# Optimization experiments

Measured on AMD Instinct MI355X. Metric: run time of the kernel, lower is better.

Reference implementation:

```python
import jax, jax.numpy as jnp
import numpy as np

B, L, D, H = 4, 2048, 512, 8
HD = D // H  # 64
MAX_REL = 4


def setup_inputs() -> dict:
    key = jax.random.key(0)
    ks = jax.random.split(key, 13)
    s = 1.0 / np.sqrt(D)
    return {
        "q": jax.random.normal(ks[0], (B, L, D), jnp.float32),
        "k": jax.random.normal(ks[1], (B, L, D), jnp.float32),
        "v": jax.random.normal(ks[2], (B, L, D), jnp.float32),
        "Wq": jax.random.normal(ks[3], (D, D), jnp.float32) * s,
        "bq": jax.random.normal(ks[4], (D,), jnp.float32) * 0.01,
        "Wk": jax.random.normal(ks[5], (D, D), jnp.float32) * s,
        "bk": jax.random.normal(ks[6], (D,), jnp.float32) * 0.01,
        "Wv": jax.random.normal(ks[7], (D, D), jnp.float32) * s,
        "bv": jax.random.normal(ks[8], (D,), jnp.float32) * 0.01,
        "Wo": jax.random.normal(ks[9], (D, D), jnp.float32) * s,
        "bo": jax.random.normal(ks[10], (D,), jnp.float32) * 0.01,
        "rel_k_table": jax.random.normal(ks[11], (2 * MAX_REL + 1, HD), jnp.float32),
        "rel_v_table": jax.random.normal(ks[12], (2 * MAX_REL + 1, HD), jnp.float32),
    }


def _to_heads(x):
    # [B, L, D] -> [B, H, L, HD]
    b, l, d = x.shape
    return x.reshape(b, l, H, d // H).transpose(0, 2, 1, 3)


def reference(q, k, v, Wq, bq, Wk, bk, Wv, bv, Wo, bo, rel_k_table, rel_v_table):
    # NOTE: in the source, the relative-attention output is overwritten by the
    # plain SDPA call immediately after, so observable math = SDPA only.
    # rel_k_table / rel_v_table are dead parameters (zero gradient).
    relu = jax.nn.relu
    qh = _to_heads(relu(q @ Wq.T + bq))  # [B,H,L,HD]
    kh = _to_heads(relu(k @ Wk.T + bk))
    vh = _to_heads(relu(v @ Wv.T + bv))
    # scale by sqrt(d_key)=sqrt(512), matching the original (not sqrt(head_dim))
    scores = jnp.einsum("bhqd,bhkd->bhqk", qh, kh) / jnp.sqrt(jnp.float32(D))
    attn = jax.nn.softmax(scores, axis=-1)
    out = jnp.einsum("bhqk,bhkd->bhqd", attn, vh)  # [B,H,L,HD]
    out = out.transpose(0, 2, 1, 3).reshape(B, L, D)
    return relu(out @ Wo.T + bo)
```

## Files before the change

kernel.cpp:

```cpp
#include <hip/hip_runtime.h>
#include <hip/hip_bf16.h>

#define B_  4
#define L_  2048
#define D_  512
#define H_  8
#define HD_ 64
#define M_  (B_ * L_)

typedef __bf16 bf16;
typedef __attribute__((ext_vector_type(8)))  __bf16 bf16x8;
typedef __attribute__((ext_vector_type(4)))  __bf16 bf16x4;
typedef __attribute__((ext_vector_type(16))) float  f32x16;

__device__ __forceinline__ f32x16 mfma32(bf16x8 a, bf16x8 b, f32x16 c) {
    return __builtin_amdgcn_mfma_f32_32x32x16_bf16(a, b, c, 0, 0, 0);
}

__device__ __forceinline__ void pack_body(const float* __restrict__ src,
                                          bf16* __restrict__ dst, int R,
                                          int m0, int k0)
{
    __shared__ __align__(16) bf16 tile[64][76];
    const int t = threadIdx.x;
#pragma unroll
    for (int rep = 0; rep < 4; rep++) {
        const int idx = rep * 256 + t;
        const int r = idx >> 4, c4 = idx & 15;
        const float4 f = *(const float4*)(src + (size_t)(m0 + r) * 512 + k0 + c4 * 4);
        bf16x4 v; v[0] = (bf16)f.x; v[1] = (bf16)f.y; v[2] = (bf16)f.z; v[3] = (bf16)f.w;
        *(bf16x4*)(&tile[r][c4 * 4]) = v;
    }
    __syncthreads();
#pragma unroll
    for (int rep = 0; rep < 2; rep++) {
        const int s = rep * 256 + t;
        const int ml = s & 63, kpl = s >> 6;
        const bf16x4 lo = *(const bf16x4*)(&tile[ml][kpl * 8]);
        const bf16x4 hi4 = *(const bf16x4*)(&tile[ml][kpl * 8 + 4]);
        bf16x8 v;
#pragma unroll
        for (int e = 0; e < 4; e++) { v[e] = lo[e]; v[e + 4] = hi4[e]; }
        *(bf16x8*)(dst + ((size_t)(k0 / 8 + kpl) * R + m0 + ml) * 8) = v;
    }
}

__global__ __launch_bounds__(256) void pack_all(
    const float* __restrict__ q, const float* __restrict__ k,
    const float* __restrict__ W0, const float* __restrict__ W1,
    const float* __restrict__ W2, const float* __restrict__ W3,
    bf16* __restrict__ Wp, bf16* __restrict__ P0, bf16* __restrict__ P1)
{
    const int z = blockIdx.z;
    if (z < 4) {
        if (blockIdx.x >= 8) return;
        const float* src = z == 0 ? W0 : z == 1 ? W1 : z == 2 ? W2 : W3;
        pack_body(src, Wp + (size_t)z * 64 * 512 * 8, 512, blockIdx.x * 64, blockIdx.y * 64);
    } else {
        pack_body(z == 4 ? q : k, z == 4 ? P0 : P1, M_, blockIdx.x * 64, blockIdx.y * 64);
    }
}

__global__ __launch_bounds__(256) void pack_x(const float* __restrict__ src,
                                              bf16* __restrict__ dst)
{
    pack_body(src, dst, M_, blockIdx.x * 64, blockIdx.y * 64);
}

struct PJob {
    const bf16* X; const bf16* W; const float* bias; void* out;
    float postmul; int mode;
};

__global__ __launch_bounds__(256) void proj_kernel(PJob j0, PJob j1)
{
    const PJob jb = (blockIdx.z == 0) ? j0 : j1;
    const int w    = threadIdx.x >> 6;
    const int lane = threadIdx.x & 63;
    const int l31  = lane & 31;
    const int hi   = lane >> 5;
    const int m0 = blockIdx.x * 128;
    const int n0 = blockIdx.y * 64;
    const int mh = w & 1;
    const int nh = w >> 1;

    __shared__ __align__(16) bf16 Ab[2][16][64][8];
    __shared__ __align__(16) bf16 Bb[2][8][64][8];

    f32x16 acc[2];
#pragma unroll
    for (int mi = 0; mi < 2; mi++)
#pragma unroll
        for (int r = 0; r < 16; r++) acc[mi][r] = 0.0f;

    auto ldA = [&](int f, int k0) -> bf16x8 {
        return *(const bf16x8*)(jb.X + ((size_t)((k0 >> 3) + (f >> 2) * 2 + hi) * M_
                                        + m0 + (f & 3) * 32 + l31) * 8);
    };
    auto ldB = [&](int f, int k0) -> bf16x8 {
        return *(const bf16x8*)(jb.W + ((size_t)((k0 >> 3) + (f >> 1) * 2 + hi) * 512
                                        + n0 + (f & 1) * 32 + l31) * 8);
    };

    bf16x8 ra[4], rb[2];
#pragma unroll
    for (int i = 0; i < 4; i++) ra[i] = ldA(w * 4 + i, 0);
#pragma unroll
    for (int i = 0; i < 2; i++) rb[i] = ldB(w * 2 + i, 0);
#pragma unroll
    for (int i = 0; i < 4; i++) *(bf16x8*)(&Ab[0][w * 4 + i][lane][0]) = ra[i];
#pragma unroll
    for (int i = 0; i < 2; i++) *(bf16x8*)(&Bb[0][w * 2 + i][lane][0]) = rb[i];
    __syncthreads();

    for (int it = 0; it < 8; it++) {
        const int cur = it & 1;
        if (it < 7) {
            const int kn = (it + 1) * 64;
#pragma unroll
            for (int i = 0; i < 4; i++) ra[i] = ldA(w * 4 + i, kn);
#pragma unroll
            for (int i = 0; i < 2; i++) rb[i] = ldB(w * 2 + i, kn);
        }
#pragma unroll
        for (int ks = 0; ks < 4; ks++) {
            const bf16x8 bfr = *(const bf16x8*)(&Bb[cur][ks * 2 + nh][lane][0]);
#pragma unroll
            for (int mi = 0; mi < 2; mi++) {
                const bf16x8 afr = *(const bf16x8*)(&Ab[cur][ks * 4 + mh * 2 + mi][lane][0]);
                acc[mi] = mfma32(afr, bfr, acc[mi]);
            }
        }
        if (it < 7) {
#pragma unroll
            for (int i = 0; i < 4; i++) *(bf16x8*)(&Ab[1 - cur][w * 4 + i][lane][0]) = ra[i];
#pragma unroll
            for (int i = 0; i < 2; i++) *(bf16x8*)(&Bb[1 - cur][w * 2 + i][lane][0]) = rb[i];
            __syncthreads();
        }
    }

    const int col = n0 + nh * 32 + l31;
    const float bn = jb.bias[col];
    const int mode = jb.mode;
#pragma unroll
    for (int mi = 0; mi < 2; mi++)
#pragma unroll
        for (int r = 0; r < 16; r++) {
            const int row = m0 + (mh * 2 + mi) * 32 + (r & 3) + 8 * (r >> 2) + 4 * hi;
            float v = fmaxf(acc[mi][r] + bn, 0.0f);
            if (mode == 2) {
                ((float*)jb.out)[(size_t)row * D_ + col] = v;
            } else {
                v *= jb.postmul;
                const int b = row >> 11, l = row & (L_ - 1);
                const int h = col >> 6,  hd = col & (HD_ - 1);
                const int bh = b * H_ + h;
                size_t idx;
                if (mode == 0) {
                    idx = ((size_t)bh * L_ + l) * HD_ + hd;
                } else if (mode == 1) {
                    idx = (((size_t)bh * 8 + (hd >> 3)) * L_ + l) * 8 + (hd & 7);
                } else {
                    const int swzl = (l & ~15) | (l & 3) | ((l & 4) << 1) | ((l & 8) >> 1);
                    idx = (((size_t)bh * 256 + (swzl >> 3)) * 64 + hd) * 8 + (swzl & 7);
                }
                ((bf16*)jb.out)[idx] = (bf16)v;
            }
        }
}

__global__ __launch_bounds__(128) void attn_kernel(
    const bf16* __restrict__ qh, const bf16* __restrict__ Kp,
    const bf16* __restrict__ Vp, bf16* __restrict__ Op)
{
    const int w    = threadIdx.x >> 6;
    const int lane = threadIdx.x & 63;
    const int l31  = lane & 31;
    const int hi   = lane >> 5;
    const int bh   = blockIdx.y;
    const int qb   = blockIdx.x * 64 + w * 32;

    const bf16* Q   = qh + (size_t)bh * L_ * HD_;
    const bf16* Kpb = Kp + (size_t)bh * 8 * L_ * 8;
    const bf16* Vpb = Vp + (size_t)bh * 256 * 64 * 8;

    __shared__ __align__(16) bf16 Kb[2][8][64][8];
    __shared__ __align__(16) bf16 Vb[2][8][64][8];
    __shared__ float Lw[2][32];

    bf16x8 qf[4];
#pragma unroll
    for (int ks = 0; ks < 4; ks++)
        qf[ks] = *(const bf16x8*)(Q + (size_t)(qb + l31) * HD_ + ks * 16 + hi * 8);

    f32x16 zz;
#pragma unroll
    for (int r = 0; r < 16; r++) zz[r] = 0.0f;
    f32x16 o0 = zz, o1 = zz;
    float lsum = 0.0f;

    const bf16* kp[4];
    const bf16* vp[4];
#pragma unroll
    for (int i = 0; i < 4; i++) {
        const int f = w * 4 + i;
        kp[i] = Kpb + ((size_t)((f >> 1) * 2 + hi) * L_ + (f & 1) * 32 + l31) * 8;
        vp[i] = Vpb + ((size_t)((f >> 1) * 2 + hi) * 64 + (f & 1) * 32 + l31) * 8;
    }

    bf16x8 kr[4], vr[4];
#pragma unroll
    for (int i = 0; i < 4; i++) {
        kr[i] = *(const bf16x8*)kp[i]; kp[i] += 512;
        vr[i] = *(const bf16x8*)vp[i]; vp[i] += 4096;
    }
#pragma unroll
    for (int i = 0; i < 4; i++) {
        *(bf16x8*)(&Kb[0][w * 4 + i][lane][0]) = kr[i];
        *(bf16x8*)(&Vb[0][w * 4 + i][lane][0]) = vr[i];
    }
    __syncthreads();

    for (int t = 0; t < 32; t++) {
        const int cur = t & 1;
        if (t < 31) {
#pragma unroll
            for (int i = 0; i < 4; i++) {
                kr[i] = *(const bf16x8*)kp[i]; kp[i] += 512;
                vr[i] = *(const bf16x8*)vp[i]; vp[i] += 4096;
            }
        }

        f32x16 s0 = mfma32(*(const bf16x8*)(&Kb[cur][0][lane][0]), qf[0], zz);
        f32x16 s1 = mfma32(*(const bf16x8*)(&Kb[cur][1][lane][0]), qf[0], zz);
#pragma unroll
        for (int ks = 1; ks < 4; ks++) {
            s0 = mfma32(*(const bf16x8*)(&Kb[cur][ks * 2 + 0][lane][0]), qf[ks], s0);
            s1 = mfma32(*(const bf16x8*)(&Kb[cur][ks * 2 + 1][lane][0]), qf[ks], s1);
        }

#pragma unroll
        for (int r = 0; r < 16; r++) {
            const float e = __builtin_amdgcn_exp2f(s0[r]);
            s0[r] = e; lsum += e;
        }
        {
            bf16x8 pf0, pf1;
#pragma unroll
            for (int u = 0; u < 8; u++) { pf0[u] = (bf16)s0[u]; pf1[u] = (bf16)s0[8 + u]; }
            o0 = mfma32(pf0, *(const bf16x8*)(&Vb[cur][0][lane][0]), o0);
            o1 = mfma32(pf0, *(const bf16x8*)(&Vb[cur][1][lane][0]), o1);
            o0 = mfma32(pf1, *(const bf16x8*)(&Vb[cur][2][lane][0]), o0);
            o1 = mfma32(pf1, *(const bf16x8*)(&Vb[cur][3][lane][0]), o1);
        }
#pragma unroll
        for (int r = 0; r < 16; r++) {
            const float e = __builtin_amdgcn_exp2f(s1[r]);
            s1[r] = e; lsum += e;
        }
        {
            bf16x8 pf2, pf3;
#pragma unroll
            for (int u = 0; u < 8; u++) { pf2[u] = (bf16)s1[u]; pf3[u] = (bf16)s1[8 + u]; }
            o0 = mfma32(pf2, *(const bf16x8*)(&Vb[cur][4][lane][0]), o0);
            o1 = mfma32(pf2, *(const bf16x8*)(&Vb[cur][5][lane][0]), o1);
            o0 = mfma32(pf3, *(const bf16x8*)(&Vb[cur][6][lane][0]), o0);
            o1 = mfma32(pf3, *(const bf16x8*)(&Vb[cur][7][lane][0]), o1);
        }

        if (t < 31) {
#pragma unroll
            for (int i = 0; i < 4; i++) {
                *(bf16x8*)(&Kb[1 - cur][w * 4 + i][lane][0]) = kr[i];
                *(bf16x8*)(&Vb[1 - cur][w * 4 + i][lane][0]) = vr[i];
            }
            __syncthreads();
        }
    }

    lsum += __shfl_xor(lsum, 32);
    if (hi == 0) Lw[w][l31] = lsum;
    asm volatile("s_waitcnt lgkmcnt(0)" ::: "memory");

    const int b = bh >> 3, h = bh & 7;
#pragma unroll
    for (int r = 0; r < 16; r++) {
        const int rl = (r & 3) + 8 * (r >> 2) + 4 * hi;
        const float inv = 1.0f / Lw[w][rl];
        const int m = b * L_ + qb + rl;
        {
            const int col = h * HD_ + l31;
            Op[((size_t)(col >> 3) * M_ + m) * 8 + (col & 7)] = (bf16)(o0[r] * inv);
        }
        {
            const int col = h * HD_ + 32 + l31;
            Op[((size_t)(col >> 3) * M_ + m) * 8 + (col & 7)] = (bf16)(o1[r] * inv);
        }
    }
}

extern "C" void kernel_launch(void* const* d_in, const int* in_sizes, int n_in,
                              void* d_out, int out_size, void* d_ws, size_t ws_size,
                              hipStream_t stream)
{
    (void)in_sizes; (void)n_in; (void)out_size; (void)ws_size;
    const float* q  = (const float*)d_in[0];
    const float* k  = (const float*)d_in[1];
    const float* v  = (const float*)d_in[2];
    const float* Wq = (const float*)d_in[3];
    const float* bq = (const float*)d_in[4];
    const float* Wk = (const float*)d_in[5];
    const float* bk = (const float*)d_in[6];
    const float* Wv = (const float*)d_in[7];
    const float* bv = (const float*)d_in[8];
    const float* Wo = (const float*)d_in[9];
    const float* bo = (const float*)d_in[10];
    float* out = (float*)d_out;

    char* ws = (char*)d_ws;
    const size_t MB = 1024 * 1024;
    bf16* P0  = (bf16*)(ws);
    bf16* P1  = (bf16*)(ws + 8 * MB);
    bf16* Wp  = (bf16*)(ws + 16 * MB);
    bf16* Vp  = (bf16*)(ws + 18 * MB);
    bf16* qh  = (bf16*)(d_out);
    bf16* Kp  = (bf16*)((char*)d_out + 8 * MB);
    bf16* Opb = P0;

    bf16* Wqp = Wp;
    bf16* Wkp = Wp + (size_t)64 * 512 * 8;
    bf16* Wvp = Wp + (size_t)2 * 64 * 512 * 8;
    bf16* Wop = Wp + (size_t)3 * 64 * 512 * 8;

    const float SCALE_LOG2E = 0.06377946282349575f;

    dim3 pb(256);
    pack_all<<<dim3(128, 8, 6), pb, 0, stream>>>(q, k, Wq, Wk, Wv, Wo, Wp, P0, P1);

    PJob jq{P0, Wqp, bq, qh, SCALE_LOG2E, 0};
    PJob jk{P1, Wkp, bk, Kp, 1.0f, 1};
    proj_kernel<<<dim3(64, 8, 2), pb, 0, stream>>>(jq, jk);

    pack_x<<<dim3(128, 8), pb, 0, stream>>>(v, P1);

    PJob jv{P1, Wvp, bv, Vp, 1.0f, 3};
    proj_kernel<<<dim3(64, 8, 1), pb, 0, stream>>>(jv, jv);

    attn_kernel<<<dim3(L_ / 64, B_ * H_), dim3(128), 0, stream>>>(qh, Kp, Vp, Opb);

    PJob jo{Opb, Wop, bo, out, 1.0f, 2};
    proj_kernel<<<dim3(64, 8, 1), pb, 0, stream>>>(jo, jo);
}
```

Measured before the change: 210.6 us.

## Deepen prefetch pipelines, load K fragments directly, compute row sums via MFMA

Packing of the v input moves into the single pack_all launch, so one kernel launch goes away. The projection GEMM gets a three-deep register prefetch ring and an occupancy hint. The attention kernel stops staging K through shared memory: each wave loads the full K fragments straight from global into registers. V gets a deeper prefetch, and the softmax denominator is accumulated with an extra MFMA against a ones vector, replacing scalar adds and the LDS reduction. This trades higher register pressure and duplicated K loads across the two waves for fewer LDS round trips and barriers, and it reorganises the workspace buffers.

```diff
diff --git a/kernel.cpp b/kernel.cpp
--- a/kernel.cpp
+++ b/kernel.cpp
@@ -47,9 +47,11 @@
 
 __global__ __launch_bounds__(256) void pack_all(
     const float* __restrict__ q, const float* __restrict__ k,
+    const float* __restrict__ v,
     const float* __restrict__ W0, const float* __restrict__ W1,
     const float* __restrict__ W2, const float* __restrict__ W3,
-    bf16* __restrict__ Wp, bf16* __restrict__ P0, bf16* __restrict__ P1)
+    bf16* __restrict__ Wp, bf16* __restrict__ P0, bf16* __restrict__ P1,
+    bf16* __restrict__ P2)
 {
     const int z = blockIdx.z;
     if (z < 4) {
@@ -57,14 +59,10 @@
         const float* src = z == 0 ? W0 : z == 1 ? W1 : z == 2 ? W2 : W3;
         pack_body(src, Wp + (size_t)z * 64 * 512 * 8, 512, blockIdx.x * 64, blockIdx.y * 64);
     } else {
-        pack_body(z == 4 ? q : k, z == 4 ? P0 : P1, M_, blockIdx.x * 64, blockIdx.y * 64);
-    }
-}
-
-__global__ __launch_bounds__(256) void pack_x(const float* __restrict__ src,
-                                              bf16* __restrict__ dst)
-{
-    pack_body(src, dst, M_, blockIdx.x * 64, blockIdx.y * 64);
+        const float* src = z == 4 ? q : z == 5 ? k : v;
+        bf16* dst = z == 4 ? P0 : z == 5 ? P1 : P2;
+        pack_body(src, dst, M_, blockIdx.x * 64, blockIdx.y * 64);
+    }
 }
 
 struct PJob {
@@ -72,7 +70,7 @@
     float postmul; int mode;
 };
 
-__global__ __launch_bounds__(256) void proj_kernel(PJob j0, PJob j1)
+__global__ __launch_bounds__(256, 3) void proj_kernel(PJob j0, PJob j1)
 {
     const PJob jb = (blockIdx.z == 0) ? j0 : j1;
     const int w    = threadIdx.x >> 6;
@@ -102,25 +100,33 @@
                                         + n0 + (f & 1) * 32 + l31) * 8);
     };
 
-    bf16x8 ra[4], rb[2];
-#pragma unroll
-    for (int i = 0; i < 4; i++) ra[i] = ldA(w * 4 + i, 0);
-#pragma unroll
-    for (int i = 0; i < 2; i++) rb[i] = ldB(w * 2 + i, 0);
-#pragma unroll
-    for (int i = 0; i < 4; i++) *(bf16x8*)(&Ab[0][w * 4 + i][lane][0]) = ra[i];
-#pragma unroll
-    for (int i = 0; i < 2; i++) *(bf16x8*)(&Bb[0][w * 2 + i][lane][0]) = rb[i];
+    bf16x8 rA[3][4], rB[3][2];
+#pragma unroll
+    for (int i = 0; i < 4; i++) rA[0][i] = ldA(w * 4 + i, 0);
+#pragma unroll
+    for (int i = 0; i < 2; i++) rB[0][i] = ldB(w * 2 + i, 0);
+#pragma unroll
+    for (int i = 0; i < 4; i++) *(bf16x8*)(&Ab[0][w * 4 + i][lane][0]) = rA[0][i];
+#pragma unroll
+    for (int i = 0; i < 2; i++) *(bf16x8*)(&Bb[0][w * 2 + i][lane][0]) = rB[0][i];
+#pragma unroll
+    for (int s = 1; s < 3; s++) {
+#pragma unroll
+        for (int i = 0; i < 4; i++) rA[s][i] = ldA(w * 4 + i, s * 64);
+#pragma unroll
+        for (int i = 0; i < 2; i++) rB[s][i] = ldB(w * 2 + i, s * 64);
+    }
     __syncthreads();
 
+#pragma unroll
     for (int it = 0; it < 8; it++) {
         const int cur = it & 1;
-        if (it < 7) {
-            const int kn = (it + 1) * 64;
-#pragma unroll
-            for (int i = 0; i < 4; i++) ra[i] = ldA(w * 4 + i, kn);
-#pragma unroll
-            for (int i = 0; i < 2; i++) rb[i] = ldB(w * 2 + i, kn);
+        if (it < 5) {
+            const int s = it % 3, kn = (it + 3) * 64;
+#pragma unroll
+            for (int i = 0; i < 4; i++) rA[s][i] = ldA(w * 4 + i, kn);
+#pragma unroll
+            for (int i = 0; i < 2; i++) rB[s][i] = ldB(w * 2 + i, kn);
         }
 #pragma unroll
         for (int ks = 0; ks < 4; ks++) {
@@ -132,10 +138,11 @@
             }
         }
         if (it < 7) {
-#pragma unroll
-            for (int i = 0; i < 4; i++) *(bf16x8*)(&Ab[1 - cur][w * 4 + i][lane][0]) = ra[i];
-#pragma unroll
-            for (int i = 0; i < 2; i++) *(bf16x8*)(&Bb[1 - cur][w * 2 + i][lane][0]) = rb[i];
+            const int s = (it + 1) % 3;
+#pragma unroll
+            for (int i = 0; i < 4; i++) *(bf16x8*)(&Ab[1 - cur][w * 4 + i][lane][0]) = rA[s][i];
+#pragma unroll
+            for (int i = 0; i < 2; i++) *(bf16x8*)(&Bb[1 - cur][w * 2 + i][lane][0]) = rB[s][i];
             __syncthreads();
         }
     }
@@ -170,7 +177,7 @@
         }
 }
 
-__global__ __launch_bounds__(128) void attn_kernel(
+__global__ __launch_bounds__(128, 2) void attn_kernel(
     const bf16* __restrict__ qh, const bf16* __restrict__ Kp,
     const bf16* __restrict__ Vp, bf16* __restrict__ Op)
 {
@@ -185,9 +192,7 @@
     const bf16* Kpb = Kp + (size_t)bh * 8 * L_ * 8;
     const bf16* Vpb = Vp + (size_t)bh * 256 * 64 * 8;
 
-    __shared__ __align__(16) bf16 Kb[2][8][64][8];
     __shared__ __align__(16) bf16 Vb[2][8][64][8];
-    __shared__ float Lw[2][32];
 
     bf16x8 qf[4];
 #pragma unroll
@@ -197,106 +202,99 @@
     f32x16 zz;
 #pragma unroll
     for (int r = 0; r < 16; r++) zz[r] = 0.0f;
-    f32x16 o0 = zz, o1 = zz;
-    float lsum = 0.0f;
-
-    const bf16* kp[4];
-    const bf16* vp[4];
-#pragma unroll
-    for (int i = 0; i < 4; i++) {
-        const int f = w * 4 + i;
-        kp[i] = Kpb + ((size_t)((f >> 1) * 2 + hi) * L_ + (f & 1) * 32 + l31) * 8;
-        vp[i] = Vpb + ((size_t)((f >> 1) * 2 + hi) * 64 + (f & 1) * 32 + l31) * 8;
-    }
-
-    bf16x8 kr[4], vr[4];
-#pragma unroll
-    for (int i = 0; i < 4; i++) {
-        kr[i] = *(const bf16x8*)kp[i]; kp[i] += 512;
-        vr[i] = *(const bf16x8*)vp[i]; vp[i] += 4096;
-    }
-#pragma unroll
-    for (int i = 0; i < 4; i++) {
-        *(bf16x8*)(&Kb[0][w * 4 + i][lane][0]) = kr[i];
-        *(bf16x8*)(&Vb[0][w * 4 + i][lane][0]) = vr[i];
-    }
+    f32x16 o0 = zz, o1 = zz, lacc = zz;
+    bf16x8 ones;
+#pragma unroll
+    for (int u = 0; u < 8; u++) ones[u] = (bf16)1.0f;
+
+    auto ldK = [&](int f, int t) -> bf16x8 {
+        return *(const bf16x8*)(Kpb + ((size_t)((f >> 1) * 2 + hi) * L_
+                                       + t * 64 + (f & 1) * 32 + l31) * 8);
+    };
+    auto ldV = [&](int f, int t) -> bf16x8 {
+        return *(const bf16x8*)(Vpb + ((size_t)(t * 8 + (f >> 1) * 2 + hi) * 64
+                                       + (f & 1) * 32 + l31) * 8);
+    };
+
+    bf16x8 kr[8], vr[2][4];
+#pragma unroll
+    for (int i = 0; i < 4; i++) vr[0][i] = ldV(w * 4 + i, 0);
+#pragma unroll
+    for (int i = 0; i < 4; i++) *(bf16x8*)(&Vb[0][w * 4 + i][lane][0]) = vr[0][i];
+#pragma unroll
+    for (int i = 0; i < 4; i++) vr[1][i] = ldV(w * 4 + i, 1);
+#pragma unroll
+    for (int i = 0; i < 4; i++) vr[0][i] = ldV(w * 4 + i, 2);
+#pragma unroll
+    for (int f = 0; f < 8; f++) kr[f] = ldK(f, 0);
     __syncthreads();
 
-    for (int t = 0; t < 32; t++) {
-        const int cur = t & 1;
+    auto tile_body = [&](int t, int cur, int nxt) {
+        f32x16 s0 = mfma32(kr[0], qf[0], zz);
+        f32x16 s1 = mfma32(kr[1], qf[0], zz);
+#pragma unroll
+        for (int ks = 1; ks < 4; ks++) {
+            s0 = mfma32(kr[ks * 2 + 0], qf[ks], s0);
+            s1 = mfma32(kr[ks * 2 + 1], qf[ks], s1);
+        }
         if (t < 31) {
 #pragma unroll
-            for (int i = 0; i < 4; i++) {
-                kr[i] = *(const bf16x8*)kp[i]; kp[i] += 512;
-                vr[i] = *(const bf16x8*)vp[i]; vp[i] += 4096;
-            }
-        }
-
-        f32x16 s0 = mfma32(*(const bf16x8*)(&Kb[cur][0][lane][0]), qf[0], zz);
-        f32x16 s1 = mfma32(*(const bf16x8*)(&Kb[cur][1][lane][0]), qf[0], zz);
-#pragma unroll
-        for (int ks = 1; ks < 4; ks++) {
-            s0 = mfma32(*(const bf16x8*)(&Kb[cur][ks * 2 + 0][lane][0]), qf[ks], s0);
-            s1 = mfma32(*(const bf16x8*)(&Kb[cur][ks * 2 + 1][lane][0]), qf[ks], s1);
-        }
-
-#pragma unroll
-        for (int r = 0; r < 16; r++) {
-            const float e = __builtin_amdgcn_exp2f(s0[r]);
-            s0[r] = e; lsum += e;
-        }
+            for (int f = 0; f < 8; f++) kr[f] = ldK(f, t + 1);
+        }
+
+#pragma unroll
+        for (int r = 0; r < 16; r++) s0[r] = __builtin_amdgcn_exp2f(s0[r]);
         {
             bf16x8 pf0, pf1;
 #pragma unroll
             for (int u = 0; u < 8; u++) { pf0[u] = (bf16)s0[u]; pf1[u] = (bf16)s0[8 + u]; }
-            o0 = mfma32(pf0, *(const bf16x8*)(&Vb[cur][0][lane][0]), o0);
-            o1 = mfma32(pf0, *(const bf16x8*)(&Vb[cur][1][lane][0]), o1);
-            o0 = mfma32(pf1, *(const bf16x8*)(&Vb[cur][2][lane][0]), o0);
-            o1 = mfma32(pf1, *(const bf16x8*)(&Vb[cur][3][lane][0]), o1);
-        }
-#pragma unroll
-        for (int r = 0; r < 16; r++) {
-            const float e = __builtin_amdgcn_exp2f(s1[r]);
-            s1[r] = e; lsum += e;
-        }
+            o0   = mfma32(pf0, *(const bf16x8*)(&Vb[cur][0][lane][0]), o0);
+            o1   = mfma32(pf0, *(const bf16x8*)(&Vb[cur][1][lane][0]), o1);
+            lacc = mfma32(pf0, ones, lacc);
+            o0   = mfma32(pf1, *(const bf16x8*)(&Vb[cur][2][lane][0]), o0);
+            o1   = mfma32(pf1, *(const bf16x8*)(&Vb[cur][3][lane][0]), o1);
+            lacc = mfma32(pf1, ones, lacc);
+        }
+#pragma unroll
+        for (int r = 0; r < 16; r++) s1[r] = __builtin_amdgcn_exp2f(s1[r]);
         {
             bf16x8 pf2, pf3;
 #pragma unroll
             for (int u = 0; u < 8; u++) { pf2[u] = (bf16)s1[u]; pf3[u] = (bf16)s1[8 + u]; }
-            o0 = mfma32(pf2, *(const bf16x8*)(&Vb[cur][4][lane][0]), o0);
-            o1 = mfma32(pf2, *(const bf16x8*)(&Vb[cur][5][lane][0]), o1);
-            o0 = mfma32(pf3, *(const bf16x8*)(&Vb[cur][6][lane][0]), o0);
-            o1 = mfma32(pf3, *(const bf16x8*)(&Vb[cur][7][lane][0]), o1);
+            o0   = mfma32(pf2, *(const bf16x8*)(&Vb[cur][4][lane][0]), o0);
+            o1   = mfma32(pf2, *(const bf16x8*)(&Vb[cur][5][lane][0]), o1);
+            lacc = mfma32(pf2, ones, lacc);
+            o0   = mfma32(pf3, *(const bf16x8*)(&Vb[cur][6][lane][0]), o0);
+            o1   = mfma32(pf3, *(const bf16x8*)(&Vb[cur][7][lane][0]), o1);
+            lacc = mfma32(pf3, ones, lacc);
         }
 
         if (t < 31) {
 #pragma unroll
-            for (int i = 0; i < 4; i++) {
-                *(bf16x8*)(&Kb[1 - cur][w * 4 + i][lane][0]) = kr[i];
-                *(bf16x8*)(&Vb[1 - cur][w * 4 + i][lane][0]) = vr[i];
-            }
+            for (int i = 0; i < 4; i++)
+                *(bf16x8*)(&Vb[1 - cur][w * 4 + i][lane][0]) = vr[nxt][i];
+            const int tn = (t + 3 < 32) ? t + 3 : 31;
+#pragma unroll
+            for (int i = 0; i < 4; i++) vr[nxt][i] = ldV(w * 4 + i, tn);
             __syncthreads();
         }
-    }
-
-    lsum += __shfl_xor(lsum, 32);
-    if (hi == 0) Lw[w][l31] = lsum;
-    asm volatile("s_waitcnt lgkmcnt(0)" ::: "memory");
+    };
+
+    for (int tt = 0; tt < 16; tt++) {
+        tile_body(2 * tt + 0, 0, 1);
+        tile_body(2 * tt + 1, 1, 0);
+    }
 
     const int b = bh >> 3, h = bh & 7;
 #pragma unroll
     for (int r = 0; r < 16; r++) {
         const int rl = (r & 3) + 8 * (r >> 2) + 4 * hi;
-        const float inv = 1.0f / Lw[w][rl];
+        const float inv = 1.0f / lacc[r];
         const int m = b * L_ + qb + rl;
-        {
-            const int col = h * HD_ + l31;
-            Op[((size_t)(col >> 3) * M_ + m) * 8 + (col & 7)] = (bf16)(o0[r] * inv);
-        }
-        {
-            const int col = h * HD_ + 32 + l31;
-            Op[((size_t)(col >> 3) * M_ + m) * 8 + (col & 7)] = (bf16)(o1[r] * inv);
-        }
+        const int c0 = h * HD_ + l31;
+        Op[((size_t)(c0 >> 3) * M_ + m) * 8 + (c0 & 7)] = (bf16)(o0[r] * inv);
+        const int c1 = c0 + 32;
+        Op[((size_t)(c1 >> 3) * M_ + m) * 8 + (c1 & 7)] = (bf16)(o1[r] * inv);
     }
 }
 
@@ -322,11 +320,12 @@
     const size_t MB = 1024 * 1024;
     bf16* P0  = (bf16*)(ws);
     bf16* P1  = (bf16*)(ws + 8 * MB);
-    bf16* Wp  = (bf16*)(ws + 16 * MB);
-    bf16* Vp  = (bf16*)(ws + 18 * MB);
+    bf16* P2  = (bf16*)(ws + 16 * MB);
+    bf16* Wp  = (bf16*)(ws + 24 * MB);
     bf16* qh  = (bf16*)(d_out);
     bf16* Kp  = (bf16*)((char*)d_out + 8 * MB);
-    bf16* Opb = P0;
+    bf16* Vp  = P0;
+    bf16* Opb = P1;
 
     bf16* Wqp = Wp;
     bf16* Wkp = Wp + (size_t)64 * 512 * 8;
@@ -336,18 +335,17 @@
     const float SCALE_LOG2E = 0.06377946282349575f;
 
     dim3 pb(256);
-    pack_all<<<dim3(128, 8, 6), pb, 0, stream>>>(q, k, Wq, Wk, Wv, Wo, Wp, P0, P1);
+    pack_all<<<dim3(128, 8, 7), pb, 0, stream>>>(q, k, v, Wq, Wk, Wv, Wo,
+                                                 Wp, P0, P1, P2);
 
     PJob jq{P0, Wqp, bq, qh, SCALE_LOG2E, 0};
     PJob jk{P1, Wkp, bk, Kp, 1.0f, 1};
     proj_kernel<<<dim3(64, 8, 2), pb, 0, stream>>>(jq, jk);
 
-    pack_x<<<dim3(128, 8), pb, 0, stream>>>(v, P1);
-
-    PJob jv{P1, Wvp, bv, Vp, 1.0f, 3};
+    PJob jv{P2, Wvp, bv, Vp, 1.0f, 3};
     proj_kernel<<<dim3(64, 8, 1), pb, 0, stream>>>(jv, jv);
 
-    attn_kernel<<<dim3(L_ / 64, B_ * H_), dim3(128), 0, stream>>>(qh, Kp, Vp, Opb);
+    attn_kernel<<<dim3(32, 32), dim3(128), 0, stream>>>(qh, Kp, Vp, Opb);
 
     PJob jo{Opb, Wop, bo, out, 1.0f, 2};
     proj_kernel<<<dim3(64, 8, 1), pb, 0, stream>>>(jo, jo);
```

After: 201.2 us. -4.4%, faster.
